# Kernel optimization log

Hardware: AMD Instinct MI355X
Metric: run time of the kernel (lower is better)

## Reference

```python
import jax, jax.numpy as jnp
import numpy as np

DIM, HID, BATCH = 64, 512, 8192


def setup_inputs() -> dict:
    key = jax.random.key(0)
    ks = jax.random.split(key, 6)
    s1 = 1.0 / np.sqrt(DIM + 1)
    s2 = 1.0 / np.sqrt(HID)
    return {
        "t": jax.random.uniform(ks[0], (1,), dtype=jnp.float32),
        "x": jax.random.normal(ks[1], (BATCH, DIM), dtype=jnp.float32),
        "W1": jax.random.normal(ks[2], (DIM + 1, HID), dtype=jnp.float32) * s1,
        "b1": jnp.zeros((HID,), jnp.float32),
        "W2": jax.random.normal(ks[3], (HID, HID), dtype=jnp.float32) * s2,
        "b2": jnp.zeros((HID,), jnp.float32),
        "W3": jax.random.normal(ks[4], (HID, DIM), dtype=jnp.float32) * s2,
        "b3": jnp.zeros((DIM,), jnp.float32),
    }


def _vf_single(ts, xs, W1, b1, W2, b2, W3, b3):
    # xs: [dim], ts: scalar. Time concatenated as extra input feature.
    h = jnp.concatenate([xs, ts[None]])          # [dim+1]
    h = jnp.tanh(h @ W1 + b1)                    # [hid]
    h = jnp.tanh(h @ W2 + b2)                    # [hid]
    return h @ W3 + b3                           # [dim]


def reference(t, x, W1, b1, W2, b2, W3, b3):
    ts = t[0]
    vf = lambda xs: _vf_single(ts, xs, W1, b1, W2, b2, W3, b3)
    v = jax.vmap(vf)(x)                                   # [B, dim]
    # Exact divergence: trace of per-sample Jacobian dv/dx.
    # (Replaces the torch per-dim autograd.grad loop with one batched jacfwd.)
    J = jax.vmap(jax.jacfwd(vf))(x)                       # [B, dim, dim]
    div = jnp.trace(J, axis1=-2, axis2=-1)                # [B]
    return (v, -div[:, None])
```

## Files before the change

### kernel.cpp

```cpp
#include <hip/hip_runtime.h>

#define DIM 64
#define HID 512
#define BATCH 8192
#define MB 32
#define NTHR 512

typedef __attribute__((ext_vector_type(8))) short short8;
typedef __attribute__((ext_vector_type(4))) float f32x4;
typedef float float4_ __attribute__((ext_vector_type(4)));

__device__ __forceinline__ unsigned short f2bf(float f) {
    union { float f; unsigned u; } v; v.f = f;
    return (unsigned short)((v.u + 0x7FFFu + ((v.u >> 16) & 1u)) >> 16);
}
__device__ __forceinline__ float tanh_fast(float x) {
    float e = __expf(2.f * x);
    return 1.f - __fdividef(2.f, e + 1.f);
}

__global__ __launch_bounds__(256) void compute_MT(const float* __restrict__ W1,
                                                  const float* __restrict__ W3,
                                                  float* __restrict__ MT) {
    int j  = ((blockIdx.x & 1) << 8) + threadIdx.x;
    int ka = blockIdx.x >> 1;
    int kb = ka + 256;
    float aa = 0.f, ab = 0.f;
#pragma unroll
    for (int i = 0; i < DIM; ++i) {
        float w1 = W1[i * HID + j];
        aa = fmaf(w1, W3[ka * DIM + i], aa);
        ab = fmaf(w1, W3[kb * DIM + i], ab);
    }
    MT[(size_t)ka * HID + j] = aa;
    MT[(size_t)kb * HID + j] = ab;
}

__global__ __launch_bounds__(256) void pack_frags(
        const float* __restrict__ t,  const float* __restrict__ W1,
        const float* __restrict__ b1, const float* __restrict__ W2,
        const float* __restrict__ W3, const float* __restrict__ MT,
        unsigned short* __restrict__ w2pk, unsigned short* __restrict__ ppk,
        unsigned short* __restrict__ w3pk, unsigned short* __restrict__ w1pk,
        float* __restrict__ c1) {
    int b = blockIdx.x;
    if (b >= 288) {
        int n = (b - 288) * 256 + threadIdx.x;
        c1[n] = fmaf(t[0], W1[DIM * HID + n], b1[n]);
        return;
    }
    int gid = b * 256 + threadIdx.x;
    int f = gid >> 6, l = gid & 63;
    if (f < 512) {
        int fi = f, n = (fi >> 4) * 16 + (l & 15), kb = (fi & 15) * 32 + (l >> 4) * 8;
        unsigned short* o = w2pk + ((size_t)(fi * 64 + l)) * 8;
#pragma unroll
        for (int e = 0; e < 8; ++e) o[e] = f2bf(W2[(size_t)(kb + e) * HID + n]);
    } else if (f < 1024) {
        int fi = f - 512, n = (fi >> 4) * 16 + (l & 15), kb = (fi & 15) * 32 + (l >> 4) * 8;
        unsigned short* o = ppk + ((size_t)(fi * 64 + l)) * 8;
#pragma unroll
        for (int e = 0; e < 8; ++e)
            o[e] = f2bf(MT[(size_t)n * HID + kb + e] * W2[(size_t)(kb + e) * HID + n]);
    } else if (f < 1088) {
        int fi = f - 1024, n = (fi >> 4) * 16 + (l & 15), kb = (fi & 15) * 32 + (l >> 4) * 8;
        unsigned short* o = w3pk + ((size_t)(fi * 64 + l)) * 8;
#pragma unroll
        for (int e = 0; e < 8; ++e) o[e] = f2bf(W3[(size_t)(kb + e) * DIM + n]);
    } else {
        int fi = f - 1088, n = (fi >> 1) * 16 + (l & 15), kb = (fi & 1) * 32 + (l >> 4) * 8;
        unsigned short* o = w1pk + ((size_t)(fi * 64 + l)) * 8;
#pragma unroll
        for (int e = 0; e < 8; ++e) o[e] = f2bf(W1[(size_t)(kb + e) * HID + n]);
    }
}

__device__ __forceinline__ int afrag_addr(int mt, int ks, int row, int kwbyte) {
    return ((((mt * 16 + ks) * 16 + row) * 64) + kwbyte) ^ ((row & 7) << 4);
}

__global__ __launch_bounds__(NTHR, 2) void fused_main(
        const float* __restrict__ x,  const float* __restrict__ c1,
        const float* __restrict__ b2, const float* __restrict__ b3,
        const unsigned short* __restrict__ w1pk, const unsigned short* __restrict__ w2pk,
        const unsigned short* __restrict__ ppk,  const unsigned short* __restrict__ w3pk,
        float* __restrict__ out) {
    __shared__ unsigned short h1s[MB * HID];
    __shared__ unsigned short d1s[MB * HID];
    __shared__ unsigned short h2s[MB * HID];
    __shared__ float wred[4][MB];

    const int tid = threadIdx.x;
    const int wave = tid >> 6;
    const int wm = wave & 1;
    const int wn = wave >> 1;
    const int l = tid & 63;
    const int g = l >> 4, lr = l & 15;
    const int s0 = blockIdx.x * MB;

    union U8 { short8 s8; unsigned short u[8]; };
    short8 ax[2];
#pragma unroll
    for (int ks = 0; ks < 2; ++ks) {
        const float* xp = x + (size_t)(s0 + wm * 16 + lr) * DIM + ks * 32 + g * 8;
        float4_ x0 = *(const float4_*)xp;
        float4_ x1 = *(const float4_*)(xp + 4);
        U8 u;
        u.u[0] = f2bf(x0.x); u.u[1] = f2bf(x0.y); u.u[2] = f2bf(x0.z); u.u[3] = f2bf(x0.w);
        u.u[4] = f2bf(x1.x); u.u[5] = f2bf(x1.y); u.u[6] = f2bf(x1.z); u.u[7] = f2bf(x1.w);
        ax[ks] = u.s8;
    }
    {
        f32x4 acc1[8];
#pragma unroll
        for (int nt = 0; nt < 8; ++nt) {
            int ntg = wn * 8 + nt;
            const short8* bw = (const short8*)w1pk + (size_t)(ntg * 2) * 64 + l;
            f32x4 a = {0.f, 0.f, 0.f, 0.f};
            a = __builtin_amdgcn_mfma_f32_16x16x32_bf16(ax[0], bw[0],  a, 0, 0, 0);
            a = __builtin_amdgcn_mfma_f32_16x16x32_bf16(ax[1], bw[64], a, 0, 0, 0);
            acc1[nt] = a;
        }
#pragma unroll
        for (int nt = 0; nt < 8; ++nt) {
            int c = (wn * 8 + nt) * 16 + lr;
            float c1v = c1[c];
            int ks = c >> 5, kwb = (c & 31) * 2;
#pragma unroll
            for (int r = 0; r < 4; ++r) {
                int row = g * 4 + r;
                float h = tanh_fast(acc1[nt][r] + c1v);
                float d = fmaf(-h, h, 1.f);
                int a0 = afrag_addr(wm, ks, row, kwb);
                *(unsigned short*)((char*)h1s + a0) = f2bf(h);
                *(unsigned short*)((char*)d1s + a0) = f2bf(d);
            }
        }
    }
    __syncthreads();

    short8 ah[16], ad[16];
#pragma unroll
    for (int ks = 0; ks < 16; ++ks) {
        int a0 = afrag_addr(wm, ks, lr, g * 16);
        ah[ks] = *(const short8*)((const char*)h1s + a0);
        ad[ks] = *(const short8*)((const char*)d1s + a0);
    }
    float divp[4] = {0.f, 0.f, 0.f, 0.f};
#pragma unroll 1
    for (int nt = 0; nt < 8; ++nt) {
        int ntg = wn * 8 + nt;
        const short8* bw = (const short8*)w2pk + (size_t)(ntg * 16) * 64 + l;
        const short8* bp = (const short8*)ppk  + (size_t)(ntg * 16) * 64 + l;
        f32x4 zacc = {0.f, 0.f, 0.f, 0.f}, sacc = {0.f, 0.f, 0.f, 0.f};
#pragma unroll
        for (int ks = 0; ks < 16; ++ks) {
            zacc = __builtin_amdgcn_mfma_f32_16x16x32_bf16(ah[ks], bw[ks * 64], zacc, 0, 0, 0);
            sacc = __builtin_amdgcn_mfma_f32_16x16x32_bf16(ad[ks], bp[ks * 64], sacc, 0, 0, 0);
        }
        int c = ntg * 16 + lr;
        float b2v = b2[c];
        int ks2 = c >> 5, kwb = (c & 31) * 2;
#pragma unroll
        for (int r = 0; r < 4; ++r) {
            int row = g * 4 + r;
            float h2 = tanh_fast(zacc[r] + b2v);
            float d2 = fmaf(-h2, h2, 1.f);
            divp[r] = fmaf(sacc[r], d2, divp[r]);
            *(unsigned short*)((char*)h2s + afrag_addr(wm, ks2, row, kwb)) = f2bf(h2);
        }
    }

#pragma unroll
    for (int off = 1; off < 16; off <<= 1) {
#pragma unroll
        for (int r = 0; r < 4; ++r) divp[r] += __shfl_xor(divp[r], off, 64);
    }
    if (lr == 0) {
#pragma unroll
        for (int r = 0; r < 4; ++r) wred[wn][wm * 16 + g * 4 + r] = divp[r];
    }
    __syncthreads();
    if (tid < MB) {
        float d = wred[0][tid] + wred[1][tid] + wred[2][tid] + wred[3][tid];
        out[(size_t)BATCH * DIM + s0 + tid] = -d;
    }

    {
        short8 a2[16];
#pragma unroll
        for (int ks = 0; ks < 16; ++ks)
            a2[ks] = *(const short8*)((const char*)h2s + afrag_addr(wm, ks, lr, g * 16));
        f32x4 acc = {0.f, 0.f, 0.f, 0.f};
        const short8* bw = (const short8*)w3pk + (size_t)(wn * 16) * 64 + l;
#pragma unroll
        for (int ks = 0; ks < 16; ++ks)
            acc = __builtin_amdgcn_mfma_f32_16x16x32_bf16(a2[ks], bw[ks * 64], acc, 0, 0, 0);
        int c = wn * 16 + lr;
        float b3v = b3[c];
#pragma unroll
        for (int r = 0; r < 4; ++r)
            out[(size_t)(s0 + wm * 16 + g * 4 + r) * DIM + c] = acc[r] + b3v;
    }
}

extern "C" void kernel_launch(void* const* d_in, const int* in_sizes, int n_in,
                              void* d_out, int out_size, void* d_ws, size_t ws_size,
                              hipStream_t stream) {
    const float* t  = (const float*)d_in[0];
    const float* x  = (const float*)d_in[1];
    const float* W1 = (const float*)d_in[2];
    const float* b1 = (const float*)d_in[3];
    const float* W2 = (const float*)d_in[4];
    const float* b2 = (const float*)d_in[5];
    const float* W3 = (const float*)d_in[6];
    const float* b3 = (const float*)d_in[7];
    float* out = (float*)d_out;

    char* ws = (char*)d_ws;
    float*          MT   = (float*)ws;
    unsigned short* w2pk = (unsigned short*)(ws + (1 << 20));
    unsigned short* ppk  = (unsigned short*)(ws + (1 << 20) + (512 << 10));
    unsigned short* w3pk = (unsigned short*)(ws + (2 << 20));
    unsigned short* w1pk = (unsigned short*)(ws + (2 << 20) + (64 << 10));
    float*          c1   = (float*)(ws + (2 << 20) + (128 << 10));

    compute_MT<<<512, 256, 0, stream>>>(W1, W3, MT);
    pack_frags<<<290, 256, 0, stream>>>(t, W1, b1, W2, W3, MT, w2pk, ppk, w3pk, w1pk, c1);
    fused_main<<<BATCH / MB, NTHR, 0, stream>>>(x, c1, b2, b3, w1pk, w2pk, ppk, w3pk, out);
}
```

Measured before the change: 40.33 us.

## Use 32x32 MFMA for layer-2 and fold MT computation into weight packing

Layer 2 moves from 16x16x32 to 32x32x16 bf16 MFMA, with each wave owning two 32-column output tiles across all 32 batch rows. A-fragments now stream from LDS per k-step instead of being held in registers, and the LDS layout becomes row-major with an XOR swizzle. The separate compute_MT kernel is removed and W1·W3^T is computed inline while packing ppk, dropping one launch and the MT round-trip through global memory. This should cut launch overhead and B-operand reload cost per FLOP, at the price of more redundant FMA work in prep and more LDS reads per MFMA.

```diff
diff --git a/kernel.cpp b/kernel.cpp
--- a/kernel.cpp
+++ b/kernel.cpp
@@ -8,7 +8,10 @@
 
 typedef __attribute__((ext_vector_type(8))) short short8;
 typedef __attribute__((ext_vector_type(4))) float f32x4;
+typedef __attribute__((ext_vector_type(16))) float f32x16;
 typedef float float4_ __attribute__((ext_vector_type(4)));
+
+#define Z16 {0.f,0.f,0.f,0.f,0.f,0.f,0.f,0.f,0.f,0.f,0.f,0.f,0.f,0.f,0.f,0.f}
 
 __device__ __forceinline__ unsigned short f2bf(float f) {
     union { float f; unsigned u; } v; v.f = f;
@@ -19,27 +22,10 @@
     return 1.f - __fdividef(2.f, e + 1.f);
 }
 
-__global__ __launch_bounds__(256) void compute_MT(const float* __restrict__ W1,
-                                                  const float* __restrict__ W3,
-                                                  float* __restrict__ MT) {
-    int j  = ((blockIdx.x & 1) << 8) + threadIdx.x;
-    int ka = blockIdx.x >> 1;
-    int kb = ka + 256;
-    float aa = 0.f, ab = 0.f;
-#pragma unroll
-    for (int i = 0; i < DIM; ++i) {
-        float w1 = W1[i * HID + j];
-        aa = fmaf(w1, W3[ka * DIM + i], aa);
-        ab = fmaf(w1, W3[kb * DIM + i], ab);
-    }
-    MT[(size_t)ka * HID + j] = aa;
-    MT[(size_t)kb * HID + j] = ab;
-}
-
-__global__ __launch_bounds__(256) void pack_frags(
+__global__ __launch_bounds__(256) void prep(
         const float* __restrict__ t,  const float* __restrict__ W1,
         const float* __restrict__ b1, const float* __restrict__ W2,
-        const float* __restrict__ W3, const float* __restrict__ MT,
+        const float* __restrict__ W3,
         unsigned short* __restrict__ w2pk, unsigned short* __restrict__ ppk,
         unsigned short* __restrict__ w3pk, unsigned short* __restrict__ w1pk,
         float* __restrict__ c1) {
@@ -52,31 +38,43 @@
     int gid = b * 256 + threadIdx.x;
     int f = gid >> 6, l = gid & 63;
     if (f < 512) {
-        int fi = f, n = (fi >> 4) * 16 + (l & 15), kb = (fi & 15) * 32 + (l >> 4) * 8;
-        unsigned short* o = w2pk + ((size_t)(fi * 64 + l)) * 8;
-#pragma unroll
-        for (int e = 0; e < 8; ++e) o[e] = f2bf(W2[(size_t)(kb + e) * HID + n]);
+        int nt = f >> 5, ks = f & 31;
+        int n = nt * 32 + (l & 31), k0 = ks * 16 + (l >> 5) * 8;
+        unsigned short* o = w2pk + (size_t)(f * 64 + l) * 8;
+#pragma unroll
+        for (int e = 0; e < 8; ++e) o[e] = f2bf(W2[(size_t)(k0 + e) * HID + n]);
     } else if (f < 1024) {
-        int fi = f - 512, n = (fi >> 4) * 16 + (l & 15), kb = (fi & 15) * 32 + (l >> 4) * 8;
-        unsigned short* o = ppk + ((size_t)(fi * 64 + l)) * 8;
-#pragma unroll
-        for (int e = 0; e < 8; ++e)
-            o[e] = f2bf(MT[(size_t)n * HID + kb + e] * W2[(size_t)(kb + e) * HID + n]);
+        int fi = f - 512;
+        int nt = fi >> 5, ks = fi & 31;
+        int n = nt * 32 + (l & 31), k0 = ks * 16 + (l >> 5) * 8;
+        float m[8] = {0.f,0.f,0.f,0.f,0.f,0.f,0.f,0.f};
+        for (int i = 0; i < DIM; ++i) {
+            float w3 = W3[(size_t)n * DIM + i];
+#pragma unroll
+            for (int e = 0; e < 8; ++e) m[e] = fmaf(W1[(size_t)i * HID + k0 + e], w3, m[e]);
+        }
+        unsigned short* o = ppk + (size_t)(fi * 64 + l) * 8;
+#pragma unroll
+        for (int e = 0; e < 8; ++e) o[e] = f2bf(W2[(size_t)(k0 + e) * HID + n] * m[e]);
     } else if (f < 1088) {
-        int fi = f - 1024, n = (fi >> 4) * 16 + (l & 15), kb = (fi & 15) * 32 + (l >> 4) * 8;
-        unsigned short* o = w3pk + ((size_t)(fi * 64 + l)) * 8;
-#pragma unroll
-        for (int e = 0; e < 8; ++e) o[e] = f2bf(W3[(size_t)(kb + e) * DIM + n]);
+        int fi = f - 1024;
+        int nt = fi >> 4, ks = fi & 15;
+        int n = nt * 16 + (l & 15), k0 = ks * 32 + (l >> 4) * 8;
+        unsigned short* o = w3pk + (size_t)(fi * 64 + l) * 8;
+#pragma unroll
+        for (int e = 0; e < 8; ++e) o[e] = f2bf(W3[(size_t)(k0 + e) * DIM + n]);
     } else {
-        int fi = f - 1088, n = (fi >> 1) * 16 + (l & 15), kb = (fi & 1) * 32 + (l >> 4) * 8;
-        unsigned short* o = w1pk + ((size_t)(fi * 64 + l)) * 8;
-#pragma unroll
-        for (int e = 0; e < 8; ++e) o[e] = f2bf(W1[(size_t)(kb + e) * HID + n]);
-    }
-}
-
-__device__ __forceinline__ int afrag_addr(int mt, int ks, int row, int kwbyte) {
-    return ((((mt * 16 + ks) * 16 + row) * 64) + kwbyte) ^ ((row & 7) << 4);
+        int fi = f - 1088;
+        int nt = fi >> 1, ks = fi & 1;
+        int n = nt * 16 + (l & 15), k0 = ks * 32 + (l >> 4) * 8;
+        unsigned short* o = w1pk + (size_t)(fi * 64 + l) * 8;
+#pragma unroll
+        for (int e = 0; e < 8; ++e) o[e] = f2bf(W1[(size_t)(k0 + e) * HID + n]);
+    }
+}
+
+__device__ __forceinline__ int lds_addr(int row, int k) {
+    return (row * 1024 + k * 2) ^ ((row & 7) << 4);
 }
 
 __global__ __launch_bounds__(NTHR, 2) void fused_main(
@@ -88,15 +86,15 @@
     __shared__ unsigned short h1s[MB * HID];
     __shared__ unsigned short d1s[MB * HID];
     __shared__ unsigned short h2s[MB * HID];
-    __shared__ float wred[4][MB];
+    __shared__ float wred[8][MB];
 
     const int tid = threadIdx.x;
-    const int wave = tid >> 6;
-    const int wm = wave & 1;
-    const int wn = wave >> 1;
+    const int w = tid >> 6;
     const int l = tid & 63;
-    const int g = l >> 4, lr = l & 15;
+    const int lr = l & 15, g = l >> 4;
+    const int wm = w & 1, wn = w >> 1;
     const int s0 = blockIdx.x * MB;
+    char* h1b = (char*)h1s; char* d1b = (char*)d1s; char* h2b = (char*)h2s;
 
     union U8 { short8 s8; unsigned short u[8]; };
     short8 ax[2];
@@ -114,8 +112,7 @@
         f32x4 acc1[8];
 #pragma unroll
         for (int nt = 0; nt < 8; ++nt) {
-            int ntg = wn * 8 + nt;
-            const short8* bw = (const short8*)w1pk + (size_t)(ntg * 2) * 64 + l;
+            const short8* bw = (const short8*)w1pk + (size_t)((wn * 8 + nt) * 2) * 64 + l;
             f32x4 a = {0.f, 0.f, 0.f, 0.f};
             a = __builtin_amdgcn_mfma_f32_16x16x32_bf16(ax[0], bw[0],  a, 0, 0, 0);
             a = __builtin_amdgcn_mfma_f32_16x16x32_bf16(ax[1], bw[64], a, 0, 0, 0);
@@ -125,77 +122,86 @@
         for (int nt = 0; nt < 8; ++nt) {
             int c = (wn * 8 + nt) * 16 + lr;
             float c1v = c1[c];
-            int ks = c >> 5, kwb = (c & 31) * 2;
 #pragma unroll
             for (int r = 0; r < 4; ++r) {
-                int row = g * 4 + r;
+                int row = wm * 16 + g * 4 + r;
                 float h = tanh_fast(acc1[nt][r] + c1v);
-                float d = fmaf(-h, h, 1.f);
-                int a0 = afrag_addr(wm, ks, row, kwb);
-                *(unsigned short*)((char*)h1s + a0) = f2bf(h);
-                *(unsigned short*)((char*)d1s + a0) = f2bf(d);
+                int a0 = lds_addr(row, c);
+                *(unsigned short*)(h1b + a0) = f2bf(h);
+                *(unsigned short*)(d1b + a0) = f2bf(fmaf(-h, h, 1.f));
             }
         }
     }
     __syncthreads();
 
-    short8 ah[16], ad[16];
-#pragma unroll
-    for (int ks = 0; ks < 16; ++ks) {
-        int a0 = afrag_addr(wm, ks, lr, g * 16);
-        ah[ks] = *(const short8*)((const char*)h1s + a0);
-        ad[ks] = *(const short8*)((const char*)d1s + a0);
-    }
-    float divp[4] = {0.f, 0.f, 0.f, 0.f};
-#pragma unroll 1
-    for (int nt = 0; nt < 8; ++nt) {
-        int ntg = wn * 8 + nt;
-        const short8* bw = (const short8*)w2pk + (size_t)(ntg * 16) * 64 + l;
-        const short8* bp = (const short8*)ppk  + (size_t)(ntg * 16) * 64 + l;
-        f32x4 zacc = {0.f, 0.f, 0.f, 0.f}, sacc = {0.f, 0.f, 0.f, 0.f};
-#pragma unroll
-        for (int ks = 0; ks < 16; ++ks) {
-            zacc = __builtin_amdgcn_mfma_f32_16x16x32_bf16(ah[ks], bw[ks * 64], zacc, 0, 0, 0);
-            sacc = __builtin_amdgcn_mfma_f32_16x16x32_bf16(ad[ks], bp[ks * 64], sacc, 0, 0, 0);
-        }
-        int c = ntg * 16 + lr;
+    const int nt0 = w * 2, nt1 = w * 2 + 1;
+    f32x16 z0 = Z16, z1 = Z16, sv0 = Z16, sv1 = Z16;
+#pragma unroll 4
+    for (int ks = 0; ks < 32; ++ks) {
+        int arow = l & 31;
+        int ab = lds_addr(arow, ks * 16 + (l >> 5) * 8);
+        short8 ah = *(const short8*)(h1b + ab);
+        short8 ad = *(const short8*)(d1b + ab);
+        const short8* bw = (const short8*)w2pk;
+        const short8* bp = (const short8*)ppk;
+        short8 bw0 = bw[(size_t)(nt0 * 32 + ks) * 64 + l];
+        short8 bw1 = bw[(size_t)(nt1 * 32 + ks) * 64 + l];
+        short8 bp0 = bp[(size_t)(nt0 * 32 + ks) * 64 + l];
+        short8 bp1 = bp[(size_t)(nt1 * 32 + ks) * 64 + l];
+        z0  = __builtin_amdgcn_mfma_f32_32x32x16_bf16(ah, bw0, z0, 0, 0, 0);
+        z1  = __builtin_amdgcn_mfma_f32_32x32x16_bf16(ah, bw1, z1, 0, 0, 0);
+        sv0 = __builtin_amdgcn_mfma_f32_32x32x16_bf16(ad, bp0, sv0, 0, 0, 0);
+        sv1 = __builtin_amdgcn_mfma_f32_32x32x16_bf16(ad, bp1, sv1, 0, 0, 0);
+    }
+
+    float divp[16];
+#pragma unroll
+    for (int r = 0; r < 16; ++r) divp[r] = 0.f;
+#pragma unroll
+    for (int j = 0; j < 2; ++j) {
+        f32x16 z  = j ? z1 : z0;
+        f32x16 sv = j ? sv1 : sv0;
+        int c = (w * 2 + j) * 32 + (l & 31);
         float b2v = b2[c];
-        int ks2 = c >> 5, kwb = (c & 31) * 2;
-#pragma unroll
-        for (int r = 0; r < 4; ++r) {
-            int row = g * 4 + r;
-            float h2 = tanh_fast(zacc[r] + b2v);
+#pragma unroll
+        for (int r = 0; r < 16; ++r) {
+            int row = (r & 3) + 8 * (r >> 2) + 4 * (l >> 5);
+            float h2 = tanh_fast(z[r] + b2v);
             float d2 = fmaf(-h2, h2, 1.f);
-            divp[r] = fmaf(sacc[r], d2, divp[r]);
-            *(unsigned short*)((char*)h2s + afrag_addr(wm, ks2, row, kwb)) = f2bf(h2);
-        }
-    }
-
-#pragma unroll
-    for (int off = 1; off < 16; off <<= 1) {
-#pragma unroll
-        for (int r = 0; r < 4; ++r) divp[r] += __shfl_xor(divp[r], off, 64);
-    }
-    if (lr == 0) {
-#pragma unroll
-        for (int r = 0; r < 4; ++r) wred[wn][wm * 16 + g * 4 + r] = divp[r];
+            divp[r] = fmaf(sv[r], d2, divp[r]);
+            *(unsigned short*)(h2b + lds_addr(row, c)) = f2bf(h2);
+        }
+    }
+
+#pragma unroll
+    for (int off = 1; off < 32; off <<= 1) {
+#pragma unroll
+        for (int r = 0; r < 16; ++r) divp[r] += __shfl_xor(divp[r], off, 64);
+    }
+    if ((l & 31) == 0) {
+#pragma unroll
+        for (int r = 0; r < 16; ++r) {
+            int row = (r & 3) + 8 * (r >> 2) + 4 * (l >> 5);
+            wred[w][row] = divp[r];
+        }
     }
     __syncthreads();
     if (tid < MB) {
-        float d = wred[0][tid] + wred[1][tid] + wred[2][tid] + wred[3][tid];
+        float d = 0.f;
+#pragma unroll
+        for (int ww = 0; ww < 8; ++ww) d += wred[ww][tid];
         out[(size_t)BATCH * DIM + s0 + tid] = -d;
     }
 
     {
-        short8 a2[16];
-#pragma unroll
-        for (int ks = 0; ks < 16; ++ks)
-            a2[ks] = *(const short8*)((const char*)h2s + afrag_addr(wm, ks, lr, g * 16));
         f32x4 acc = {0.f, 0.f, 0.f, 0.f};
         const short8* bw = (const short8*)w3pk + (size_t)(wn * 16) * 64 + l;
 #pragma unroll
-        for (int ks = 0; ks < 16; ++ks)
-            acc = __builtin_amdgcn_mfma_f32_16x16x32_bf16(a2[ks], bw[ks * 64], acc, 0, 0, 0);
+        for (int ks = 0; ks < 16; ++ks) {
+            int ab = lds_addr(wm * 16 + lr, ks * 32 + g * 8);
+            short8 a2 = *(const short8*)(h2b + ab);
+            acc = __builtin_amdgcn_mfma_f32_16x16x32_bf16(a2, bw[ks * 64], acc, 0, 0, 0);
+        }
         int c = wn * 16 + lr;
         float b3v = b3[c];
 #pragma unroll
@@ -218,14 +224,12 @@
     float* out = (float*)d_out;
 
     char* ws = (char*)d_ws;
-    float*          MT   = (float*)ws;
-    unsigned short* w2pk = (unsigned short*)(ws + (1 << 20));
-    unsigned short* ppk  = (unsigned short*)(ws + (1 << 20) + (512 << 10));
-    unsigned short* w3pk = (unsigned short*)(ws + (2 << 20));
-    unsigned short* w1pk = (unsigned short*)(ws + (2 << 20) + (64 << 10));
-    float*          c1   = (float*)(ws + (2 << 20) + (128 << 10));
-
-    compute_MT<<<512, 256, 0, stream>>>(W1, W3, MT);
-    pack_frags<<<290, 256, 0, stream>>>(t, W1, b1, W2, W3, MT, w2pk, ppk, w3pk, w1pk, c1);
+    unsigned short* w2pk = (unsigned short*)ws;
+    unsigned short* ppk  = (unsigned short*)(ws + (512 << 10));
+    unsigned short* w3pk = (unsigned short*)(ws + (1 << 20));
+    unsigned short* w1pk = (unsigned short*)(ws + (1 << 20) + (64 << 10));
+    float*          c1   = (float*)(ws + (1 << 20) + (128 << 10));
+
+    prep<<<290, 256, 0, stream>>>(t, W1, b1, W2, W3, w2pk, ppk, w3pk, w1pk, c1);
     fused_main<<<BATCH / MB, NTHR, 0, stream>>>(x, c1, b2, b3, w1pk, w2pk, ppk, w3pk, out);
 }
```

After: 36.95 us. -8.4%, faster.
